# Kernel tuning notes

Measured on AMD Instinct MI355X. Metric: run time of the kernel, lower is better.

Reference implementation:

```python
import jax, jax.numpy as jnp
import numpy as np

B, N, D_V, D_MODEL, D_FF, N_HEADS = 32, 64, 6, 128, 512, 8


def _ln(x, g, b):
    m = x.mean(-1, keepdims=True)
    v = ((x - m) ** 2).mean(-1, keepdims=True)
    return (x - m) / jnp.sqrt(v + 1e-5) * g + b


def _mha(q_in, k_in, v_in, mask, Wq, Wk, Wv, Wo):
    # mask: (b, Lq, Lk) bool, True = attend
    b, Lq, D = q_in.shape
    H, dh = N_HEADS, D_MODEL // N_HEADS
    q = (q_in @ Wq).reshape(b, Lq, H, dh)
    k = (k_in @ Wk).reshape(b, k_in.shape[1], H, dh)
    v = (v_in @ Wv).reshape(b, v_in.shape[1], H, dh)
    s = jnp.einsum('bqhd,bkhd->bhqk', q, k) / (dh ** 0.5)
    s = jnp.where(mask[:, None, :, :], s, -1e9)
    o = jnp.einsum('bhqk,bkhd->bqhd', jax.nn.softmax(s, axis=-1), v).reshape(b, Lq, D)
    return o @ Wo


def setup_inputs() -> dict:
    key = jax.random.key(0)
    ks = jax.random.split(key, 40)
    def p(i, shape, scale=0.05):
        return jax.random.normal(ks[i], shape, dtype=jnp.float32) * scale
    nm = jax.random.randint(ks[1], (B, N, N), 0, 2, dtype=jnp.int32)
    nm = nm.at[:, jnp.arange(N), jnp.arange(N)].set(1)  # self always a neighbor
    inp = {
        'agent_infos': jax.random.normal(ks[0], (B, N, N, D_V), dtype=jnp.float32),
        'neighbor_masks': nm,
        'padding_mask': jnp.ones((B, N), dtype=jnp.int32),
        'is_from_my_env': jnp.ones((B,), dtype=jnp.int32),
        # src_embed
        'W_emb': p(2, (D_V, D_MODEL)), 'b_emb': jnp.zeros((D_MODEL,), jnp.float32),
        # encoder layer (self-attn + FFN, post-LN)
        'Wq': p(3, (D_MODEL, D_MODEL)), 'Wk': p(4, (D_MODEL, D_MODEL)),
        'Wv': p(5, (D_MODEL, D_MODEL)), 'Wo': p(6, (D_MODEL, D_MODEL)),
        'ln1_g': jnp.ones((D_MODEL,), jnp.float32), 'ln1_b': jnp.zeros((D_MODEL,), jnp.float32),
        'W1': p(7, (D_MODEL, D_FF)), 'b1': jnp.zeros((D_FF,), jnp.float32),
        'W2': p(8, (D_FF, D_MODEL)), 'b2': jnp.zeros((D_MODEL,), jnp.float32),
        'ln2_g': jnp.ones((D_MODEL,), jnp.float32), 'ln2_b': jnp.zeros((D_MODEL,), jnp.float32),
        # decoder layer (cross-attn + FFN, post-LN)
        'Uq': p(9, (D_MODEL, D_MODEL)), 'Uk': p(10, (D_MODEL, D_MODEL)),
        'Uv': p(11, (D_MODEL, D_MODEL)), 'Uo': p(12, (D_MODEL, D_MODEL)),
        'ln3_g': jnp.ones((D_MODEL,), jnp.float32), 'ln3_b': jnp.zeros((D_MODEL,), jnp.float32),
        'W3': p(13, (D_MODEL, D_FF)), 'b3': jnp.zeros((D_FF,), jnp.float32),
        'W4': p(14, (D_FF, D_MODEL)), 'b4': jnp.zeros((D_MODEL,), jnp.float32),
        'ln4_g': jnp.ones((D_MODEL,), jnp.float32), 'ln4_b': jnp.zeros((D_MODEL,), jnp.float32),
        # generator (single-head query/key scorer)
        'Wg_q': p(15, (D_MODEL, D_MODEL)), 'Wg_k': p(16, (D_MODEL, D_MODEL)),
    }
    return inp


def reference(agent_infos, neighbor_masks, padding_mask, is_from_my_env,
              W_emb, b_emb, Wq, Wk, Wv, Wo, ln1_g, ln1_b, W1, b1, W2, b2, ln2_g, ln2_b,
              Uq, Uk, Uv, Uo, ln3_g, ln3_b, W3, b3, W4, b4, ln4_g, ln4_b, Wg_q, Wg_k):
    # Fold the per-agent python loop of the original into the batch dim: BN = B * N.
    src = agent_infos.reshape(B * N, N, D_V)
    neigh = neighbor_masks.reshape(B * N, N) != 0           # True = neighbor (attendable)
    x = src @ W_emb + b_emb                                 # (BN, N, D)
    src_mask = neigh[:, :, None] & neigh[:, None, :]        # (BN, N, N)
    x = _ln(x + _mha(x, x, x, src_mask, Wq, Wk, Wv, Wo), ln1_g, ln1_b)
    x = _ln(x + (jax.nn.relu(x @ W1 + b1) @ W2 + b2), ln2_g, ln2_b)
    # context vector -- faithful to the original get_context_vector (which sums rows
    # where pad_tokens==True, i.e. NON-neighbors, and divides by the neighbor count)
    pad = (~neigh)[:, :, None].astype(x.dtype)
    cnt = neigh.sum(axis=1).reshape(-1, 1, 1).astype(x.dtype)
    h_c = (x * pad).sum(axis=1, keepdims=True) / cnt        # (BN, 1, D)
    stm = neigh[:, None, :]                                 # src_tgt_mask (BN, 1, N)
    y = _ln(h_c + _mha(h_c, x, x, stm, Uq, Uk, Uv, Uo), ln3_g, ln3_b)
    y = _ln(y + (jax.nn.relu(y @ W3 + b3) @ W4 + b4), ln4_g, ln4_b)
    logits = jnp.einsum('bqd,bkd->bqk', y @ Wg_q, x @ Wg_k) / (D_MODEL ** 0.5)
    probs = jnp.where(stm, jax.nn.sigmoid(logits), 0.0)[:, 0, :]   # (BN, N)
    att_scores = probs.reshape(B, N, N)
    num_agents = padding_mask.sum(axis=1).astype(x.dtype).reshape(B, 1, 1)
    avg_h_c_N = h_c.reshape(B, N, D_MODEL).sum(axis=1, keepdims=True) / num_agents
    return att_scores, avg_h_c_N
```

## Files before the change

### kernel.cpp

```cpp
#include <hip/hip_runtime.h>
#include <hip/hip_bf16.h>
#include <math.h>

#define ITEMS 2048
#define SEQ   64
#define DM    128
#define DFF   512
#define ATT_OFF 131072

typedef unsigned short u16;
typedef __attribute__((ext_vector_type(4))) unsigned short ushort4v;
typedef __attribute__((ext_vector_type(8))) short short8v;
typedef __attribute__((ext_vector_type(4))) float float4v;

#define MFMA16(a,b,c) __builtin_amdgcn_mfma_f32_16x16x32_bf16(a,b,c,0,0,0)

#define XST 136
#define VST 72
#define PST 76

#define XS_B   0
#define QS_B   17408
#define KS_B   34816
#define VT_B   52224
#define PL_B   70656
#define ZB_B   80384
#define PF_B   80400
#define CNT_B  80656
#define NA_B   80660
#define NB_B   80664
#define ARENA_SZ 80672

#define HC_B   (KS_B+0)
#define QV_B   (KS_B+512)
#define OV_B   (KS_B+1024)
#define YV_B   (KS_B+1536)
#define Y2_B   (KS_B+2048)
#define GW_B   (KS_B+2560)
#define WALL_B (VT_B+0)
#define SALL_B (VT_B+4096)
#define PALL_B (VT_B+6144)
#define TALL_B (VT_B+8192)
#define FF_B   (VT_B+12288)
#define W4P_B  (VT_B+14336)

#define WQ_O   0
#define WK_O   16384
#define WV_O   32768
#define WO_O   49152
#define UK_O   65536
#define UV_O   81920
#define W1_O   98304
#define W2_O   163840
#define UQ_O   229376
#define UO_O   245760
#define WGQ_O  262144
#define WGK_O  278528
#define W3_O   294912
#define W4_O   360448
#define WS_TOT 425984

__device__ __forceinline__ u16 f2b(float f){
  union { float f; unsigned u; } v; v.f = f;
  unsigned r = (v.u + 0x7fffu + ((v.u >> 16) & 1u)) >> 16;
  return (u16)r;
}
__device__ __forceinline__ float b2f(u16 h){
  union { unsigned u; float f; } v; v.u = ((unsigned)h) << 16;
  return v.f;
}
__device__ __forceinline__ float wsum(float v){
  #pragma unroll
  for (int off = 1; off < 64; off <<= 1) v += __shfl_xor(v, off);
  return v;
}
__device__ __forceinline__ void ln_vec(float* v, const float* g, const float* b, int lane){
  float v0 = v[lane], v1 = v[lane+64];
  float m  = wsum(v0+v1) * (1.f/128.f);
  float d0 = v0-m, d1 = v1-m;
  float var = wsum(d0*d0+d1*d1) * (1.f/128.f);
  float inv = rsqrtf(var + 1e-5f);
  v[lane]    = d0*inv*g[lane]    + b[lane];
  v[lane+64] = d1*inv*g[lane+64] + b[lane+64];
}
__device__ __forceinline__ float dot128(const u16* __restrict__ wrow, const float* __restrict__ x){
  const short8v* wr = (const short8v*)wrow;
  float a = 0.f;
  #pragma unroll
  for (int c8 = 0; c8 < 16; c8++){
    short8v v = wr[c8];
    #pragma unroll
    for (int q = 0; q < 8; q++) a += b2f((u16)v[q]) * x[c8*8+q];
  }
  return a;
}

__global__ void prep_all(const float* __restrict__ Wq, const float* __restrict__ Wk,
                         const float* __restrict__ Wv, const float* __restrict__ Wo,
                         const float* __restrict__ Uk, const float* __restrict__ Uv,
                         const float* __restrict__ W1, const float* __restrict__ W2,
                         const float* __restrict__ Uq, const float* __restrict__ Uo,
                         const float* __restrict__ Wgq, const float* __restrict__ Wgk,
                         const float* __restrict__ W3, const float* __restrict__ W4,
                         u16* __restrict__ wts){
  int idx = blockIdx.x*256 + threadIdx.x;
  if (idx >= WS_TOT) return;
  float v;
  if (idx < 98304){
    int wsel = idx >> 14, r = idx & 16383;
    const float* tab[6] = {Wq,Wk,Wv,Wo,Uk,Uv};
    int o = r >> 7, i = r & 127;
    v = tab[wsel][i*128 + o];
  } else if (idx < W2_O){
    int r = idx - W1_O; int o = r >> 7, i = r & 127;
    v = W1[i*512 + o];
  } else if (idx < UQ_O){
    int r = idx - W2_O; int o = r >> 9, i = r & 511;
    v = W2[i*128 + o];
  } else if (idx < UO_O){
    int r = idx - UQ_O; int o = r >> 7, i = r & 127;
    v = Uq[i*128 + o];
  } else if (idx < WGQ_O){
    int r = idx - UO_O; int o = r >> 7, i = r & 127;
    v = Uo[i*128 + o];
  } else if (idx < WGK_O){
    int r = idx - WGQ_O; int o = r >> 7, i = r & 127;
    v = Wgq[i*128 + o];
  } else if (idx < W3_O){
    v = Wgk[idx - WGK_O];
  } else if (idx < W4_O){
    int r = idx - W3_O; int j = r >> 7, e = r & 127;
    v = W3[e*512 + j];
  } else {
    int r = idx - W4_O; int o = r >> 9, j = r & 511;
    v = W4[j*128 + o];
  }
  wts[idx] = f2b(v);
}

__global__ void init_avg(float* __restrict__ out){
  out[ATT_OFF + blockIdx.x*256 + threadIdx.x] = 0.f;
}

__global__ __launch_bounds__(256, 2) void vicsek_fused(
    const float* __restrict__ agent_infos,
    const int*   __restrict__ nmask,
    const int*   __restrict__ pmask,
    const u16*   __restrict__ wts,
    const float* __restrict__ W_emb, const float* __restrict__ b_emb,
    const float* __restrict__ ln1g,  const float* __restrict__ ln1b,
    const float* __restrict__ b1,    const float* __restrict__ b2,
    const float* __restrict__ ln2g,  const float* __restrict__ ln2b,
    const float* __restrict__ ln3g,  const float* __restrict__ ln3b,
    const float* __restrict__ b3,    const float* __restrict__ b4,
    const float* __restrict__ ln4g,  const float* __restrict__ ln4b,
    float* __restrict__ out)
{
  __shared__ __align__(16) char arena[ARENA_SZ];
  u16* Xs = (u16*)(arena + XS_B);
  u16* Qs = (u16*)(arena + QS_B);
  u16* Ks = (u16*)(arena + KS_B);
  u16* VT = (u16*)(arena + VT_B);
  u16* Pl = (u16*)(arena + PL_B);
  u16* zb = (u16*)(arena + ZB_B);
  float* padf  = (float*)(arena + PF_B);
  float* cnt_s = (float*)(arena + CNT_B);
  float* na_s  = (float*)(arena + NA_B);
  unsigned long long* nb_s = (unsigned long long*)(arena + NB_B);

  const int item = blockIdx.x;
  const int tid  = threadIdx.x;
  const int lane = tid & 63;
  const int w    = tid >> 6;
  const int row0 = w*16;
  const int arow = lane & 15;
  const int akg  = lane >> 4;

  const u16* WqT = wts + WQ_O;  const u16* WkT = wts + WK_O;
  const u16* WvT = wts + WV_O;  const u16* WoT = wts + WO_O;
  const u16* UkT = wts + UK_O;  const u16* UvT = wts + UV_O;
  const u16* W1T = wts + W1_O;  const u16* W2T = wts + W2_O;
  const u16* UqT = wts + UQ_O;  const u16* UoT = wts + UO_O;
  const u16* WgqT = wts + WGQ_O; const u16* WgkB = wts + WGK_O;
  const u16* W3T = wts + W3_O;  const u16* W4T = wts + W4_O;

  if (w == 0){
    int m = nmask[item*SEQ + lane];
    padf[lane] = m ? 0.f : 1.f;
    float c = wsum(m ? 1.f : 0.f);
    unsigned long long bb = __ballot(m != 0);
    if (lane == 0){ cnt_s[0] = c; nb_s[0] = bb; }
  }
  if (w == 1){
    float na = wsum((float)pmask[(item>>6)*SEQ + lane]);
    if (lane == 0) na_s[0] = na;
  }
  if (tid < 8) zb[tid] = 0;

  const float* src = agent_infos + (size_t)item*SEQ*6;
  for (int e = tid; e < SEQ*DM; e += 256){
    int r = e >> 7, c = e & 127;
    float a = b_emb[c];
    #pragma unroll
    for (int k = 0; k < 6; k++) a += src[r*6+k]*W_emb[k*DM+c];
    Xs[r*XST + c] = f2b(a);
  }
  __syncthreads();

  const unsigned long long nbits = nb_s[0];

  short8v aX[4];
  #pragma unroll
  for (int k = 0; k < 4; k++) aX[k] = *(const short8v*)(Xs + (row0+arow)*XST + k*32 + akg*8);

  for (int t = 0; t < 8; t++){
    const u16* wq = WqT + (t*16+arow)*128 + akg*8;
    const u16* wk = WkT + (t*16+arow)*128 + akg*8;
    const u16* wv = WvT + (t*16+arow)*128 + akg*8;
    float4v cq = {0,0,0,0}, ck = {0,0,0,0}, cv = {0,0,0,0};
    #pragma unroll
    for (int k = 0; k < 4; k++){
      cq = MFMA16(aX[k], *(const short8v*)(wq + k*32), cq);
      ck = MFMA16(aX[k], *(const short8v*)(wk + k*32), ck);
      cv = MFMA16(*(const short8v*)(wv + k*32), aX[k], cv);
    }
    #pragma unroll
    for (int i = 0; i < 4; i++){
      Qs[(row0+akg*4+i)*XST + t*16+arow] = f2b(cq[i]);
      Ks[(row0+akg*4+i)*XST + t*16+arow] = f2b(ck[i]);
      VT[(t*16+akg*4+i)*VST + row0+arow] = f2b(cv[i]);
    }
  }
  float4v accW[8];
  #pragma unroll
  for (int t = 0; t < 8; t++)
    #pragma unroll
    for (int i = 0; i < 4; i++)
      accW[t][i] = b2f(Xs[(row0+akg*4+i)*XST + t*16 + arow]);
  __syncthreads();

  for (int h = 0; h < 8; h++){
    const u16* qp = (akg < 2) ? (Qs + (row0+arow)*XST + h*16 + akg*8) : zb;
    short8v bq = *(const short8v*)qp;
    float4v st[4];
    #pragma unroll
    for (int kb = 0; kb < 4; kb++){
      const u16* kp = (akg < 2) ? (Ks + (kb*16+arow)*XST + h*16 + akg*8) : zb;
      float4v z = {0,0,0,0};
      st[kb] = MFMA16(*(const short8v*)kp, bq, z);
    }
    bool qok = (nbits >> (row0+arow)) & 1ull;
    float pr[16]; float mx = -3.0e38f;
    #pragma unroll
    for (int kb = 0; kb < 4; kb++)
      #pragma unroll
      for (int i = 0; i < 4; i++){
        int key = kb*16 + akg*4 + i;
        float s = st[kb][i]*0.25f;
        if (!qok || !((nbits>>key)&1ull)) s = -1.0e9f;
        pr[kb*4+i] = s; mx = fmaxf(mx, s);
      }
    mx = fmaxf(mx, __shfl_xor(mx,16)); mx = fmaxf(mx, __shfl_xor(mx,32));
    float sum = 0.f;
    #pragma unroll
    for (int z = 0; z < 16; z++){ pr[z] = __expf(pr[z]-mx); sum += pr[z]; }
    sum += __shfl_xor(sum,16); sum += __shfl_xor(sum,32);
    float inv = 1.f/sum;
    #pragma unroll
    for (int kb = 0; kb < 4; kb++)
      #pragma unroll
      for (int i = 0; i < 4; i++)
        Pl[(kb*16+akg*4+i)*PST + row0+arow] = f2b(pr[kb*4+i]*inv);
    float4v ot = {0,0,0,0};
    #pragma unroll
    for (int c2 = 0; c2 < 2; c2++){
      short8v av = *(const short8v*)(VT + (h*16+arow)*VST + c2*32 + akg*8);
      short8v bp;
      #pragma unroll
      for (int j = 0; j < 8; j++) bp[j] = (short)Pl[(c2*32+akg*8+j)*PST + row0+arow];
      ot = MFMA16(av, bp, ot);
    }
    ushort4v ov4;
    #pragma unroll
    for (int i = 0; i < 4; i++) ov4[i] = f2b(ot[i]);
    *(ushort4v*)(Xs + (row0+arow)*XST + h*16 + akg*4) = ov4;
  }

  {
    short8v aO[4];
    #pragma unroll
    for (int k = 0; k < 4; k++) aO[k] = *(const short8v*)(Xs + (row0+arow)*XST + k*32 + akg*8);
    #pragma unroll
    for (int k = 0; k < 4; k++)
      #pragma unroll
      for (int t = 0; t < 8; t++)
        accW[t] = MFMA16(aO[k], *(const short8v*)(WoT + (t*16+arow)*128 + k*32 + akg*8), accW[t]);
    float g8[8], bb8[8];
    #pragma unroll
    for (int t = 0; t < 8; t++){ g8[t] = ln1g[t*16+arow]; bb8[t] = ln1b[t*16+arow]; }
    #pragma unroll
    for (int i = 0; i < 4; i++){
      float sm = 0.f;
      #pragma unroll
      for (int t = 0; t < 8; t++) sm += accW[t][i];
      sm += __shfl_xor(sm,1); sm += __shfl_xor(sm,2); sm += __shfl_xor(sm,4); sm += __shfl_xor(sm,8);
      float mean = sm*(1.f/128.f);
      float vs = 0.f;
      #pragma unroll
      for (int t = 0; t < 8; t++){ float d = accW[t][i]-mean; vs += d*d; }
      vs += __shfl_xor(vs,1); vs += __shfl_xor(vs,2); vs += __shfl_xor(vs,4); vs += __shfl_xor(vs,8);
      float inv = rsqrtf(vs*(1.f/128.f) + 1e-5f);
      #pragma unroll
      for (int t = 0; t < 8; t++)
        Xs[(row0+akg*4+i)*XST + t*16 + arow] = f2b((accW[t][i]-mean)*inv*g8[t] + bb8[t]);
    }
  }
  #pragma unroll
  for (int k = 0; k < 4; k++) aX[k] = *(const short8v*)(Xs + (row0+arow)*XST + k*32 + akg*8);

  {
    u16* Hb = Qs;
    float4v accY[8];
    #pragma unroll
    for (int t = 0; t < 8; t++){
      float bb = b2[t*16 + arow];
      #pragma unroll
      for (int i = 0; i < 4; i++)
        accY[t][i] = bb + b2f(Xs[(row0+akg*4+i)*XST + t*16 + arow]);
    }
    for (int c = 0; c < 4; c++){
      #pragma unroll
      for (int t = 0; t < 8; t++){
        float bb = b1[c*128 + t*16 + arow];
        float4v acc = {bb,bb,bb,bb};
        #pragma unroll
        for (int k = 0; k < 4; k++)
          acc = MFMA16(aX[k], *(const short8v*)(W1T + (c*128+t*16+arow)*128 + k*32 + akg*8), acc);
        #pragma unroll
        for (int i = 0; i < 4; i++)
          Hb[(row0+akg*4+i)*XST + t*16 + arow] = f2b(fmaxf(acc[i], 0.f));
      }
      #pragma unroll
      for (int k = 0; k < 4; k++){
        short8v aH = *(const short8v*)(Hb + (row0+arow)*XST + k*32 + akg*8);
        #pragma unroll
        for (int t = 0; t < 8; t++)
          accY[t] = MFMA16(aH, *(const short8v*)(W2T + (t*16+arow)*512 + c*128 + k*32 + akg*8), accY[t]);
      }
    }
    float g8[8], bb8[8];
    #pragma unroll
    for (int t = 0; t < 8; t++){ g8[t] = ln2g[t*16+arow]; bb8[t] = ln2b[t*16+arow]; }
    #pragma unroll
    for (int i = 0; i < 4; i++){
      float sm = 0.f;
      #pragma unroll
      for (int t = 0; t < 8; t++) sm += accY[t][i];
      sm += __shfl_xor(sm,1); sm += __shfl_xor(sm,2); sm += __shfl_xor(sm,4); sm += __shfl_xor(sm,8);
      float mean = sm*(1.f/128.f);
      float vs = 0.f;
      #pragma unroll
      for (int t = 0; t < 8; t++){ float d = accY[t][i]-mean; vs += d*d; }
      vs += __shfl_xor(vs,1); vs += __shfl_xor(vs,2); vs += __shfl_xor(vs,4); vs += __shfl_xor(vs,8);
      float inv = rsqrtf(vs*(1.f/128.f) + 1e-5f);
      #pragma unroll
      for (int t = 0; t < 8; t++)
        Xs[(row0+akg*4+i)*XST + t*16 + arow] = f2b((accY[t][i]-mean)*inv*g8[t] + bb8[t]);
    }
  }
  __syncthreads();

  float* hc   = (float*)(arena + HC_B);
  float* qv   = (float*)(arena + QV_B);
  float* ov   = (float*)(arena + OV_B);
  float* yv   = (float*)(arena + YV_B);
  float* y2   = (float*)(arena + Y2_B);
  float* gw   = (float*)(arena + GW_B);
  float* wall = (float*)(arena + WALL_B);
  float* sall = (float*)(arena + SALL_B);
  float* pall = (float*)(arena + PALL_B);
  float* tall = (float*)(arena + TALL_B);
  float* ff   = (float*)(arena + FF_B);
  float* w4p  = (float*)(arena + W4P_B);

  if (tid < DM){
    float a = 0.f;
    #pragma unroll 8
    for (int r = 0; r < SEQ; r++) a += b2f(Xs[r*XST + tid]) * padf[r];
    a /= cnt_s[0];
    hc[tid] = a;
    atomicAdd(&out[ATT_OFF + (item>>6)*DM + tid], a/na_s[0]);
  }
  __syncthreads();

  if (tid < DM) qv[tid] = dot128(UqT + tid*128, hc);
  __syncthreads();
  if (tid < DM){
    #pragma unroll
    for (int h = 0; h < 8; h++){
      float a = 0.f;
      #pragma unroll
      for (int d = 0; d < 16; d++) a += b2f(UkT[(h*16+d)*128 + tid]) * qv[h*16+d];
      wall[h*128 + tid] = a;
    }
  }
  __syncthreads();
  for (int idx = tid; idx < 512; idx += 256){
    int h = idx >> 6, j = idx & 63;
    const short8v* xr = (const short8v*)(Xs + j*XST);
    const float* wv_ = wall + h*128;
    float a = 0.f;
    #pragma unroll
    for (int c8 = 0; c8 < 16; c8++){
      short8v v = xr[c8];
      #pragma unroll
      for (int q = 0; q < 8; q++) a += b2f((u16)v[q]) * wv_[c8*8+q];
    }
    sall[idx] = a*0.25f;
  }
  __syncthreads();
  for (int hh = w; hh < 8; hh += 4){
    float s = sall[hh*64 + lane];
    if (!((nbits>>lane)&1ull)) s = -1.0e9f;
    float mxx = s;
    #pragma unroll
    for (int off = 1; off < 64; off <<= 1) mxx = fmaxf(mxx, __shfl_xor(mxx, off));
    float p = __expf(s - mxx);
    float su = wsum(p);
    pall[hh*64 + lane] = p/su;
  }
  __syncthreads();
  {
    int task = tid >> 1, jh = tid & 1;
    int h = task >> 4, c8 = task & 15;
    float acc8[8] = {0,0,0,0,0,0,0,0};
    #pragma unroll 4
    for (int jj = 0; jj < 32; jj++){
      int j = jh*32 + jj;
      short8v v = *(const short8v*)(Xs + j*XST + c8*8);
      float pj = pall[h*64 + j];
      #pragma unroll
      for (int q = 0; q < 8; q++) acc8[q] += pj * b2f((u16)v[q]);
    }
    #pragma unroll
    for (int q = 0; q < 8; q++) acc8[q] += __shfl_xor(acc8[q], 1);
    if (jh == 0){
      #pragma unroll
      for (int q = 0; q < 8; q++) tall[h*128 + c8*8 + q] = acc8[q];
    }
  }
  __syncthreads();
  if (tid < DM) ov[tid] = dot128(UvT + tid*128, tall + (tid>>4)*128);
  __syncthreads();
  if (tid < DM) yv[tid] = hc[tid] + dot128(UoT + tid*128, ov);
  __syncthreads();
  if (w == 0) ln_vec(yv, ln3g, ln3b, lane);
  __syncthreads();

  for (int j = tid; j < DFF; j += 256)
    ff[j] = fmaxf(b3[j] + dot128(W3T + j*128, yv), 0.f);
  __syncthreads();
  {
    int o = tid & 127, half = tid >> 7;
    const short8v* wr = (const short8v*)(W4T + o*512 + half*256);
    const float* fh = ff + half*256;
    float a = 0.f;
    #pragma unroll
    for (int c8 = 0; c8 < 32; c8++){
      short8v v = wr[c8];
      #pragma unroll
      for (int q = 0; q < 8; q++) a += b2f((u16)v[q]) * fh[c8*8+q];
    }
    w4p[tid] = a;
  }
  __syncthreads();
  if (tid < DM) y2[tid] = b4[tid] + yv[tid] + w4p[tid] + w4p[tid+128];
  __syncthreads();
  if (w == 0) ln_vec(y2, ln4g, ln4b, lane);
  __syncthreads();

  if (tid < DM) qv[tid] = dot128(WgqT + tid*128, y2);
  __syncthreads();
  if (tid < DM) gw[tid] = dot128(WgkB + tid*128, qv);
  __syncthreads();
  if (tid < SEQ){
    float a = dot128(Xs + tid*XST, gw) ;
    a *= 0.08838834764831845f;
    out[(size_t)item*SEQ + tid] = ((nbits>>tid)&1ull) ? (1.f/(1.f+__expf(-a))) : 0.f;
  }
}

extern "C" void kernel_launch(void* const* d_in, const int* in_sizes, int n_in,
                              void* d_out, int out_size, void* d_ws, size_t ws_size,
                              hipStream_t stream)
{
  const float* agent_infos = (const float*)d_in[0];
  const int*   nmask       = (const int*)  d_in[1];
  const int*   pmask       = (const int*)  d_in[2];
  const float* W_emb = (const float*)d_in[4];
  const float* b_emb = (const float*)d_in[5];
  const float* Wq    = (const float*)d_in[6];
  const float* Wk    = (const float*)d_in[7];
  const float* Wv    = (const float*)d_in[8];
  const float* Wo    = (const float*)d_in[9];
  const float* ln1g  = (const float*)d_in[10];
  const float* ln1b  = (const float*)d_in[11];
  const float* W1    = (const float*)d_in[12];
  const float* b1    = (const float*)d_in[13];
  const float* W2    = (const float*)d_in[14];
  const float* b2    = (const float*)d_in[15];
  const float* ln2g  = (const float*)d_in[16];
  const float* ln2b  = (const float*)d_in[17];
  const float* Uq    = (const float*)d_in[18];
  const float* Uk    = (const float*)d_in[19];
  const float* Uv    = (const float*)d_in[20];
  const float* Uo    = (const float*)d_in[21];
  const float* ln3g  = (const float*)d_in[22];
  const float* ln3b  = (const float*)d_in[23];
  const float* W3    = (const float*)d_in[24];
  const float* b3    = (const float*)d_in[25];
  const float* W4    = (const float*)d_in[26];
  const float* b4    = (const float*)d_in[27];
  const float* ln4g  = (const float*)d_in[28];
  const float* ln4b  = (const float*)d_in[29];
  const float* Wgq   = (const float*)d_in[30];
  const float* Wgk   = (const float*)d_in[31];

  float* out = (float*)d_out;
  u16*   wts = (u16*)d_ws;

  prep_all<<<(WS_TOT+255)/256, 256, 0, stream>>>(Wq, Wk, Wv, Wo, Uk, Uv, W1, W2,
                                                 Uq, Uo, Wgq, Wgk, W3, W4, wts);
  init_avg<<<16, 256, 0, stream>>>(out);
  vicsek_fused<<<ITEMS, 256, 0, stream>>>(
      agent_infos, nmask, pmask, wts, W_emb, b_emb,
      ln1g, ln1b, b1, b2, ln2g, ln2b, ln3g, ln3b,
      b3, b4, ln4g, ln4b, out);
}
```

Measured before the change: 636.1 us.

## Repartition GEMMs by output columns per wave and shrink LDS for higher occupancy

Each wave now owns a slice of output columns across all 64 rows instead of a 16-row slice across all columns. Weight fragments are loaded once into registers and reused across the four row groups, which cuts repeated global/L2 weight reads. Attention runs in two batches of four heads with smaller Q/K/V staging buffers, so the LDS arena shrinks and launch bounds rise to 4 blocks per CU. The cost is extra __syncthreads, LayerNorm moved to a separate bf16 round-trip through LDS (adding rounding before normalisation), and tighter register limits that could cause spills.

```diff
diff --git a/kernel.cpp b/kernel.cpp
--- a/kernel.cpp
+++ b/kernel.cpp
@@ -9,40 +9,41 @@
 #define ATT_OFF 131072
 
 typedef unsigned short u16;
-typedef __attribute__((ext_vector_type(4))) unsigned short ushort4v;
 typedef __attribute__((ext_vector_type(8))) short short8v;
 typedef __attribute__((ext_vector_type(4))) float float4v;
 
 #define MFMA16(a,b,c) __builtin_amdgcn_mfma_f32_16x16x32_bf16(a,b,c,0,0,0)
 
-#define XST 136
-#define VST 72
-#define PST 76
+#define XST  136
+#define QST4 68
+#define VST4 70
+#define PST  76
 
 #define XS_B   0
-#define QS_B   17408
-#define KS_B   34816
-#define VT_B   52224
-#define PL_B   70656
-#define ZB_B   80384
-#define PF_B   80400
-#define CNT_B  80656
-#define NA_B   80660
-#define NB_B   80664
-#define ARENA_SZ 80672
-
-#define HC_B   (KS_B+0)
-#define QV_B   (KS_B+512)
-#define OV_B   (KS_B+1024)
-#define YV_B   (KS_B+1536)
-#define Y2_B   (KS_B+2048)
-#define GW_B   (KS_B+2560)
-#define WALL_B (VT_B+0)
-#define SALL_B (VT_B+4096)
-#define PALL_B (VT_B+6144)
-#define TALL_B (VT_B+8192)
-#define FF_B   (VT_B+12288)
-#define W4P_B  (VT_B+14336)
+#define Q4_B   17408
+#define K4_B   26112
+#define V4_B   34816
+#define PL_B   43776
+#define ZB_B   53504
+#define PF_B   53520
+#define NB_B   53776
+#define CNT_B  53784
+#define NA_B   53788
+#define ARENA_SZ 53792
+
+#define CB_B   Q4_B
+#define HC_B   17408
+#define QV_B   17920
+#define OV_B   18432
+#define YV_B   18944
+#define Y2_B   19456
+#define GW_B   19968
+#define WALL_B 20480
+#define SALL_B 24576
+#define PALL_B 26624
+#define TALL_B 28672
+#define FF_B   32768
+#define W4P_B  34816
 
 #define WQ_O   0
 #define WK_O   16384
@@ -142,7 +143,7 @@
   out[ATT_OFF + blockIdx.x*256 + threadIdx.x] = 0.f;
 }
 
-__global__ __launch_bounds__(256, 2) void vicsek_fused(
+__global__ __launch_bounds__(256, 4) void vicsek_fused(
     const float* __restrict__ agent_infos,
     const int*   __restrict__ nmask,
     const int*   __restrict__ pmask,
@@ -158,9 +159,10 @@
 {
   __shared__ __align__(16) char arena[ARENA_SZ];
   u16* Xs = (u16*)(arena + XS_B);
-  u16* Qs = (u16*)(arena + QS_B);
-  u16* Ks = (u16*)(arena + KS_B);
-  u16* VT = (u16*)(arena + VT_B);
+  u16* Q4 = (u16*)(arena + Q4_B);
+  u16* K4 = (u16*)(arena + K4_B);
+  u16* V4 = (u16*)(arena + V4_B);
+  u16* Cb = (u16*)(arena + CB_B);
   u16* Pl = (u16*)(arena + PL_B);
   u16* zb = (u16*)(arena + ZB_B);
   float* padf  = (float*)(arena + PF_B);
@@ -209,164 +211,229 @@
 
   const unsigned long long nbits = nb_s[0];
 
-  short8v aX[4];
+  float4v accW[2][4];
   #pragma unroll
-  for (int k = 0; k < 4; k++) aX[k] = *(const short8v*)(Xs + (row0+arow)*XST + k*32 + akg*8);
-
-  for (int t = 0; t < 8; t++){
-    const u16* wq = WqT + (t*16+arow)*128 + akg*8;
-    const u16* wk = WkT + (t*16+arow)*128 + akg*8;
-    const u16* wv = WvT + (t*16+arow)*128 + akg*8;
-    float4v cq = {0,0,0,0}, ck = {0,0,0,0}, cv = {0,0,0,0};
+  for (int tt = 0; tt < 2; tt++)
+    #pragma unroll
+    for (int rg = 0; rg < 4; rg++)
+      #pragma unroll
+      for (int i = 0; i < 4; i++)
+        accW[tt][rg][i] = b2f(Xs[(rg*16+akg*4+i)*XST + (2*w+tt)*16 + arow]);
+
+  auto stage_batch = [&](int b){
+    int hh = 4*b + w;
+    short8v bq[4], bk[4], bv[4];
     #pragma unroll
     for (int k = 0; k < 4; k++){
-      cq = MFMA16(aX[k], *(const short8v*)(wq + k*32), cq);
-      ck = MFMA16(aX[k], *(const short8v*)(wk + k*32), ck);
-      cv = MFMA16(*(const short8v*)(wv + k*32), aX[k], cv);
-    }
-    #pragma unroll
-    for (int i = 0; i < 4; i++){
-      Qs[(row0+akg*4+i)*XST + t*16+arow] = f2b(cq[i]);
-      Ks[(row0+akg*4+i)*XST + t*16+arow] = f2b(ck[i]);
-      VT[(t*16+akg*4+i)*VST + row0+arow] = f2b(cv[i]);
-    }
-  }
-  float4v accW[8];
+      bq[k] = *(const short8v*)(WqT + (hh*16+arow)*128 + k*32 + akg*8);
+      bk[k] = *(const short8v*)(WkT + (hh*16+arow)*128 + k*32 + akg*8);
+      bv[k] = *(const short8v*)(WvT + (hh*16+arow)*128 + k*32 + akg*8);
+    }
+    #pragma unroll
+    for (int rg = 0; rg < 4; rg++){
+      float4v cq = {0,0,0,0}, ck = {0,0,0,0}, cv = {0,0,0,0};
+      #pragma unroll
+      for (int k = 0; k < 4; k++){
+        short8v a = *(const short8v*)(Xs + (rg*16+arow)*XST + k*32 + akg*8);
+        cq = MFMA16(a, bq[k], cq);
+        ck = MFMA16(a, bk[k], ck);
+        cv = MFMA16(a, bv[k], cv);
+      }
+      #pragma unroll
+      for (int i = 0; i < 4; i++){
+        int r = rg*16 + akg*4 + i;
+        Q4[r*QST4 + w*16 + arow] = f2b(cq[i]);
+        K4[r*QST4 + w*16 + arow] = f2b(ck[i]);
+        V4[r*VST4 + w*16 + arow] = f2b(cv[i]);
+      }
+    }
+  };
+
+  auto heads_batch = [&](float4v* ocp){
+    #pragma unroll
+    for (int l = 0; l < 4; l++){
+      const u16* qp = (akg < 2) ? (Q4 + (row0+arow)*QST4 + l*16 + akg*8) : zb;
+      short8v bq = *(const short8v*)qp;
+      float4v st[4];
+      #pragma unroll
+      for (int kb = 0; kb < 4; kb++){
+        const u16* kp = (akg < 2) ? (K4 + (kb*16+arow)*QST4 + l*16 + akg*8) : zb;
+        float4v z = {0,0,0,0};
+        st[kb] = MFMA16(*(const short8v*)kp, bq, z);
+      }
+      bool qok = (nbits >> (row0+arow)) & 1ull;
+      float pr[16]; float mx = -3.0e38f;
+      #pragma unroll
+      for (int kb = 0; kb < 4; kb++)
+        #pragma unroll
+        for (int i = 0; i < 4; i++){
+          int key = kb*16 + akg*4 + i;
+          float s = st[kb][i]*0.25f;
+          if (!qok || !((nbits>>key)&1ull)) s = -1.0e9f;
+          pr[kb*4+i] = s; mx = fmaxf(mx, s);
+        }
+      mx = fmaxf(mx, __shfl_xor(mx,16)); mx = fmaxf(mx, __shfl_xor(mx,32));
+      float sum = 0.f;
+      #pragma unroll
+      for (int z2 = 0; z2 < 16; z2++){ pr[z2] = __expf(pr[z2]-mx); sum += pr[z2]; }
+      sum += __shfl_xor(sum,16); sum += __shfl_xor(sum,32);
+      float inv = 1.f/sum;
+      #pragma unroll
+      for (int kb = 0; kb < 4; kb++)
+        #pragma unroll
+        for (int i = 0; i < 4; i++)
+          Pl[(kb*16+akg*4+i)*PST + row0+arow] = f2b(pr[kb*4+i]*inv);
+      float4v o = {0,0,0,0};
+      #pragma unroll
+      for (int c2 = 0; c2 < 2; c2++){
+        short8v pa, bv;
+        #pragma unroll
+        for (int j = 0; j < 8; j++){
+          int key = c2*32 + akg*8 + j;
+          pa[j] = (short)Pl[key*PST + row0+arow];
+          bv[j] = (short)V4[key*VST4 + l*16 + arow];
+        }
+        o = MFMA16(pa, bv, o);
+      }
+      ocp[l] = o;
+    }
+  };
+
+  float4v ocA[4], ocB[4];
+  stage_batch(0);
+  __syncthreads();
+  heads_batch(ocA);
+  __syncthreads();
+  stage_batch(1);
+  __syncthreads();
   #pragma unroll
-  for (int t = 0; t < 8; t++)
+  for (int l = 0; l < 4; l++)
     #pragma unroll
     for (int i = 0; i < 4; i++)
-      accW[t][i] = b2f(Xs[(row0+akg*4+i)*XST + t*16 + arow]);
-  __syncthreads();
-
-  for (int h = 0; h < 8; h++){
-    const u16* qp = (akg < 2) ? (Qs + (row0+arow)*XST + h*16 + akg*8) : zb;
-    short8v bq = *(const short8v*)qp;
-    float4v st[4];
-    #pragma unroll
-    for (int kb = 0; kb < 4; kb++){
-      const u16* kp = (akg < 2) ? (Ks + (kb*16+arow)*XST + h*16 + akg*8) : zb;
-      float4v z = {0,0,0,0};
-      st[kb] = MFMA16(*(const short8v*)kp, bq, z);
-    }
-    bool qok = (nbits >> (row0+arow)) & 1ull;
-    float pr[16]; float mx = -3.0e38f;
-    #pragma unroll
-    for (int kb = 0; kb < 4; kb++)
-      #pragma unroll
-      for (int i = 0; i < 4; i++){
-        int key = kb*16 + akg*4 + i;
-        float s = st[kb][i]*0.25f;
-        if (!qok || !((nbits>>key)&1ull)) s = -1.0e9f;
-        pr[kb*4+i] = s; mx = fmaxf(mx, s);
+      Xs[(row0+akg*4+i)*XST + l*16 + arow] = f2b(ocA[l][i]);
+  heads_batch(ocB);
+  #pragma unroll
+  for (int l = 0; l < 4; l++)
+    #pragma unroll
+    for (int i = 0; i < 4; i++)
+      Xs[(row0+akg*4+i)*XST + (4+l)*16 + arow] = f2b(ocB[l][i]);
+  __syncthreads();
+
+  {
+    short8v bWo[2][4];
+    #pragma unroll
+    for (int tt = 0; tt < 2; tt++)
+      #pragma unroll
+      for (int k = 0; k < 4; k++)
+        bWo[tt][k] = *(const short8v*)(WoT + ((2*w+tt)*16+arow)*128 + k*32 + akg*8);
+    #pragma unroll
+    for (int k = 0; k < 4; k++)
+      #pragma unroll
+      for (int rg = 0; rg < 4; rg++){
+        short8v a = *(const short8v*)(Xs + (rg*16+arow)*XST + k*32 + akg*8);
+        #pragma unroll
+        for (int tt = 0; tt < 2; tt++)
+          accW[tt][rg] = MFMA16(a, bWo[tt][k], accW[tt][rg]);
       }
-    mx = fmaxf(mx, __shfl_xor(mx,16)); mx = fmaxf(mx, __shfl_xor(mx,32));
-    float sum = 0.f;
-    #pragma unroll
-    for (int z = 0; z < 16; z++){ pr[z] = __expf(pr[z]-mx); sum += pr[z]; }
-    sum += __shfl_xor(sum,16); sum += __shfl_xor(sum,32);
-    float inv = 1.f/sum;
-    #pragma unroll
-    for (int kb = 0; kb < 4; kb++)
-      #pragma unroll
-      for (int i = 0; i < 4; i++)
-        Pl[(kb*16+akg*4+i)*PST + row0+arow] = f2b(pr[kb*4+i]*inv);
-    float4v ot = {0,0,0,0};
-    #pragma unroll
-    for (int c2 = 0; c2 < 2; c2++){
-      short8v av = *(const short8v*)(VT + (h*16+arow)*VST + c2*32 + akg*8);
-      short8v bp;
-      #pragma unroll
-      for (int j = 0; j < 8; j++) bp[j] = (short)Pl[(c2*32+akg*8+j)*PST + row0+arow];
-      ot = MFMA16(av, bp, ot);
-    }
-    ushort4v ov4;
-    #pragma unroll
-    for (int i = 0; i < 4; i++) ov4[i] = f2b(ot[i]);
-    *(ushort4v*)(Xs + (row0+arow)*XST + h*16 + akg*4) = ov4;
-  }
+    #pragma unroll
+    for (int tt = 0; tt < 2; tt++)
+      #pragma unroll
+      for (int rg = 0; rg < 4; rg++)
+        #pragma unroll
+        for (int i = 0; i < 4; i++)
+          Cb[(rg*16+akg*4+i)*XST + (2*w+tt)*16 + arow] = f2b(accW[tt][rg][i]);
+  }
+  __syncthreads();
+  for (int rr = 0; rr < 16; rr++){
+    int r = row0 + rr;
+    float v0 = b2f(Cb[r*XST+lane]), v1 = b2f(Cb[r*XST+lane+64]);
+    float m  = wsum(v0+v1) * (1.f/128.f);
+    float d0 = v0-m, d1 = v1-m;
+    float var = wsum(d0*d0+d1*d1) * (1.f/128.f);
+    float inv = rsqrtf(var + 1e-5f);
+    Xs[r*XST+lane]    = f2b(d0*inv*ln1g[lane]    + ln1b[lane]);
+    Xs[r*XST+lane+64] = f2b(d1*inv*ln1g[lane+64] + ln1b[lane+64]);
+  }
+  __syncthreads();
 
   {
-    short8v aO[4];
-    #pragma unroll
-    for (int k = 0; k < 4; k++) aO[k] = *(const short8v*)(Xs + (row0+arow)*XST + k*32 + akg*8);
-    #pragma unroll
-    for (int k = 0; k < 4; k++)
-      #pragma unroll
-      for (int t = 0; t < 8; t++)
-        accW[t] = MFMA16(aO[k], *(const short8v*)(WoT + (t*16+arow)*128 + k*32 + akg*8), accW[t]);
-    float g8[8], bb8[8];
-    #pragma unroll
-    for (int t = 0; t < 8; t++){ g8[t] = ln1g[t*16+arow]; bb8[t] = ln1b[t*16+arow]; }
-    #pragma unroll
-    for (int i = 0; i < 4; i++){
-      float sm = 0.f;
-      #pragma unroll
-      for (int t = 0; t < 8; t++) sm += accW[t][i];
-      sm += __shfl_xor(sm,1); sm += __shfl_xor(sm,2); sm += __shfl_xor(sm,4); sm += __shfl_xor(sm,8);
-      float mean = sm*(1.f/128.f);
-      float vs = 0.f;
-      #pragma unroll
-      for (int t = 0; t < 8; t++){ float d = accW[t][i]-mean; vs += d*d; }
-      vs += __shfl_xor(vs,1); vs += __shfl_xor(vs,2); vs += __shfl_xor(vs,4); vs += __shfl_xor(vs,8);
-      float inv = rsqrtf(vs*(1.f/128.f) + 1e-5f);
-      #pragma unroll
-      for (int t = 0; t < 8; t++)
-        Xs[(row0+akg*4+i)*XST + t*16 + arow] = f2b((accW[t][i]-mean)*inv*g8[t] + bb8[t]);
-    }
-  }
-  #pragma unroll
-  for (int k = 0; k < 4; k++) aX[k] = *(const short8v*)(Xs + (row0+arow)*XST + k*32 + akg*8);
-
-  {
-    u16* Hb = Qs;
-    float4v accY[8];
-    #pragma unroll
-    for (int t = 0; t < 8; t++){
-      float bb = b2[t*16 + arow];
-      #pragma unroll
-      for (int i = 0; i < 4; i++)
-        accY[t][i] = bb + b2f(Xs[(row0+akg*4+i)*XST + t*16 + arow]);
+    u16* Hb = Cb;
+    float4v accY[2][4];
+    #pragma unroll
+    for (int tt = 0; tt < 2; tt++){
+      float bb = b2[(2*w+tt)*16 + arow];
+      #pragma unroll
+      for (int rg = 0; rg < 4; rg++)
+        #pragma unroll
+        for (int i = 0; i < 4; i++)
+          accY[tt][rg][i] = bb + b2f(Xs[(rg*16+akg*4+i)*XST + (2*w+tt)*16 + arow]);
     }
     for (int c = 0; c < 4; c++){
-      #pragma unroll
-      for (int t = 0; t < 8; t++){
-        float bb = b1[c*128 + t*16 + arow];
-        float4v acc = {bb,bb,bb,bb};
+      short8v bW1[2][4];
+      #pragma unroll
+      for (int tt = 0; tt < 2; tt++)
         #pragma unroll
         for (int k = 0; k < 4; k++)
-          acc = MFMA16(aX[k], *(const short8v*)(W1T + (c*128+t*16+arow)*128 + k*32 + akg*8), acc);
+          bW1[tt][k] = *(const short8v*)(W1T + (c*128 + w*32 + tt*16 + arow)*128 + k*32 + akg*8);
+      float4v hid[2][4];
+      #pragma unroll
+      for (int tt = 0; tt < 2; tt++){
+        float bb = b1[c*128 + w*32 + tt*16 + arow];
+        #pragma unroll
+        for (int rg = 0; rg < 4; rg++){ hid[tt][rg][0]=bb; hid[tt][rg][1]=bb; hid[tt][rg][2]=bb; hid[tt][rg][3]=bb; }
+      }
+      #pragma unroll
+      for (int k = 0; k < 4; k++)
+        #pragma unroll
+        for (int rg = 0; rg < 4; rg++){
+          short8v a = *(const short8v*)(Xs + (rg*16+arow)*XST + k*32 + akg*8);
+          #pragma unroll
+          for (int tt = 0; tt < 2; tt++)
+            hid[tt][rg] = MFMA16(a, bW1[tt][k], hid[tt][rg]);
+        }
+      #pragma unroll
+      for (int tt = 0; tt < 2; tt++)
+        #pragma unroll
+        for (int rg = 0; rg < 4; rg++)
+          #pragma unroll
+          for (int i = 0; i < 4; i++)
+            Hb[(rg*16+akg*4+i)*XST + w*32 + tt*16 + arow] = f2b(fmaxf(hid[tt][rg][i], 0.f));
+      __syncthreads();
+      short8v bW2[2][4];
+      #pragma unroll
+      for (int tt = 0; tt < 2; tt++)
+        #pragma unroll
+        for (int k = 0; k < 4; k++)
+          bW2[tt][k] = *(const short8v*)(W2T + (w*32 + tt*16 + arow)*512 + c*128 + k*32 + akg*8);
+      #pragma unroll
+      for (int k = 0; k < 4; k++)
+        #pragma unroll
+        for (int rg = 0; rg < 4; rg++){
+          short8v aH = *(const short8v*)(Hb + (rg*16+arow)*XST + k*32 + akg*8);
+          #pragma unroll
+          for (int tt = 0; tt < 2; tt++)
+            accY[tt][rg] = MFMA16(aH, bW2[tt][k], accY[tt][rg]);
+        }
+      __syncthreads();
+    }
+    #pragma unroll
+    for (int tt = 0; tt < 2; tt++)
+      #pragma unroll
+      for (int rg = 0; rg < 4; rg++)
         #pragma unroll
         for (int i = 0; i < 4; i++)
-          Hb[(row0+akg*4+i)*XST + t*16 + arow] = f2b(fmaxf(acc[i], 0.f));
-      }
-      #pragma unroll
-      for (int k = 0; k < 4; k++){
-        short8v aH = *(const short8v*)(Hb + (row0+arow)*XST + k*32 + akg*8);
-        #pragma unroll
-        for (int t = 0; t < 8; t++)
-          accY[t] = MFMA16(aH, *(const short8v*)(W2T + (t*16+arow)*512 + c*128 + k*32 + akg*8), accY[t]);
-      }
-    }
-    float g8[8], bb8[8];
-    #pragma unroll
-    for (int t = 0; t < 8; t++){ g8[t] = ln2g[t*16+arow]; bb8[t] = ln2b[t*16+arow]; }
-    #pragma unroll
-    for (int i = 0; i < 4; i++){
-      float sm = 0.f;
-      #pragma unroll
-      for (int t = 0; t < 8; t++) sm += accY[t][i];
-      sm += __shfl_xor(sm,1); sm += __shfl_xor(sm,2); sm += __shfl_xor(sm,4); sm += __shfl_xor(sm,8);
-      float mean = sm*(1.f/128.f);
-      float vs = 0.f;
-      #pragma unroll
-      for (int t = 0; t < 8; t++){ float d = accY[t][i]-mean; vs += d*d; }
-      vs += __shfl_xor(vs,1); vs += __shfl_xor(vs,2); vs += __shfl_xor(vs,4); vs += __shfl_xor(vs,8);
-      float inv = rsqrtf(vs*(1.f/128.f) + 1e-5f);
-      #pragma unroll
-      for (int t = 0; t < 8; t++)
-        Xs[(row0+akg*4+i)*XST + t*16 + arow] = f2b((accY[t][i]-mean)*inv*g8[t] + bb8[t]);
-    }
+          Cb[(rg*16+akg*4+i)*XST + (2*w+tt)*16 + arow] = f2b(accY[tt][rg][i]);
+  }
+  __syncthreads();
+  for (int rr = 0; rr < 16; rr++){
+    int r = row0 + rr;
+    float v0 = b2f(Cb[r*XST+lane]), v1 = b2f(Cb[r*XST+lane+64]);
+    float m  = wsum(v0+v1) * (1.f/128.f);
+    float d0 = v0-m, d1 = v1-m;
+    float var = wsum(d0*d0+d1*d1) * (1.f/128.f);
+    float inv = rsqrtf(var + 1e-5f);
+    Xs[r*XST+lane]    = f2b(d0*inv*ln2g[lane]    + ln2b[lane]);
+    Xs[r*XST+lane+64] = f2b(d1*inv*ln2g[lane+64] + ln2b[lane+64]);
   }
   __syncthreads();
 
@@ -484,7 +551,7 @@
   if (tid < DM) gw[tid] = dot128(WgkB + tid*128, qv);
   __syncthreads();
   if (tid < SEQ){
-    float a = dot128(Xs + tid*XST, gw) ;
+    float a = dot128(Xs + tid*XST, gw);
     a *= 0.08838834764831845f;
     out[(size_t)item*SEQ + tid] = ((nbits>>tid)&1ull) ? (1.f/(1.f+__expf(-a))) : 0.f;
   }
```

Measured after the change: 722.7 us. 13.6% more time.

## Split self-attention QKV staging into two head batches to shrink LDS and raise occupancy

Applied to the files above, without the earlier changes.

The Q/K/V projection now runs in two batches of four heads. Each batch is staged into smaller LDS buffers and attended before the next batch is computed. This roughly cuts the shared-memory arena from about 80KB to about 54KB, so launch bounds can ask for 3 blocks per CU instead of 2. The cost is two extra block-wide barriers, a tighter register budget, and overlaid scratch offsets that could alias if any are wrong.

```diff
diff --git a/kernel.cpp b/kernel.cpp
--- a/kernel.cpp
+++ b/kernel.cpp
@@ -15,34 +15,36 @@
 
 #define MFMA16(a,b,c) __builtin_amdgcn_mfma_f32_16x16x32_bf16(a,b,c,0,0,0)
 
-#define XST 136
-#define VST 72
-#define PST 76
+#define XST  136
+#define QST4 72
+#define VST4 72
+#define PST  68
 
 #define XS_B   0
-#define QS_B   17408
-#define KS_B   34816
-#define VT_B   52224
-#define PL_B   70656
-#define ZB_B   80384
-#define PF_B   80400
-#define CNT_B  80656
-#define NA_B   80660
-#define NB_B   80664
-#define ARENA_SZ 80672
-
-#define HC_B   (KS_B+0)
-#define QV_B   (KS_B+512)
-#define OV_B   (KS_B+1024)
-#define YV_B   (KS_B+1536)
-#define Y2_B   (KS_B+2048)
-#define GW_B   (KS_B+2560)
-#define WALL_B (VT_B+0)
-#define SALL_B (VT_B+4096)
-#define PALL_B (VT_B+6144)
-#define TALL_B (VT_B+8192)
-#define FF_B   (VT_B+12288)
-#define W4P_B  (VT_B+14336)
+#define Q4_B   17408
+#define K4_B   26624
+#define V4_B   35840
+#define PL_B   45056
+#define ZB_B   53760
+#define PF_B   53776
+#define NB_B   54032
+#define CNT_B  54040
+#define NA_B   54044
+#define ARENA_SZ 54048
+
+#define HB_B   Q4_B
+#define HC_B   17408
+#define QV_B   17920
+#define OV_B   18432
+#define YV_B   18944
+#define Y2_B   19456
+#define GW_B   19968
+#define WALL_B 20480
+#define SALL_B 24576
+#define PALL_B 26624
+#define TALL_B 28672
+#define FF_B   35840
+#define W4P_B  37888
 
 #define WQ_O   0
 #define WK_O   16384
@@ -142,7 +144,7 @@
   out[ATT_OFF + blockIdx.x*256 + threadIdx.x] = 0.f;
 }
 
-__global__ __launch_bounds__(256, 2) void vicsek_fused(
+__global__ __launch_bounds__(256, 3) void vicsek_fused(
     const float* __restrict__ agent_infos,
     const int*   __restrict__ nmask,
     const int*   __restrict__ pmask,
@@ -157,12 +159,12 @@
     float* __restrict__ out)
 {
   __shared__ __align__(16) char arena[ARENA_SZ];
-  u16* Xs = (u16*)(arena + XS_B);
-  u16* Qs = (u16*)(arena + QS_B);
-  u16* Ks = (u16*)(arena + KS_B);
-  u16* VT = (u16*)(arena + VT_B);
-  u16* Pl = (u16*)(arena + PL_B);
-  u16* zb = (u16*)(arena + ZB_B);
+  u16* Xs  = (u16*)(arena + XS_B);
+  u16* Q4  = (u16*)(arena + Q4_B);
+  u16* K4  = (u16*)(arena + K4_B);
+  u16* VT4 = (u16*)(arena + V4_B);
+  u16* Pl  = (u16*)(arena + PL_B);
+  u16* zb  = (u16*)(arena + ZB_B);
   float* padf  = (float*)(arena + PF_B);
   float* cnt_s = (float*)(arena + CNT_B);
   float* na_s  = (float*)(arena + NA_B);
@@ -213,78 +215,94 @@
   #pragma unroll
   for (int k = 0; k < 4; k++) aX[k] = *(const short8v*)(Xs + (row0+arow)*XST + k*32 + akg*8);
 
-  for (int t = 0; t < 8; t++){
-    const u16* wq = WqT + (t*16+arow)*128 + akg*8;
-    const u16* wk = WkT + (t*16+arow)*128 + akg*8;
-    const u16* wv = WvT + (t*16+arow)*128 + akg*8;
-    float4v cq = {0,0,0,0}, ck = {0,0,0,0}, cv = {0,0,0,0};
-    #pragma unroll
-    for (int k = 0; k < 4; k++){
-      cq = MFMA16(aX[k], *(const short8v*)(wq + k*32), cq);
-      ck = MFMA16(aX[k], *(const short8v*)(wk + k*32), ck);
-      cv = MFMA16(*(const short8v*)(wv + k*32), aX[k], cv);
-    }
-    #pragma unroll
-    for (int i = 0; i < 4; i++){
-      Qs[(row0+akg*4+i)*XST + t*16+arow] = f2b(cq[i]);
-      Ks[(row0+akg*4+i)*XST + t*16+arow] = f2b(ck[i]);
-      VT[(t*16+akg*4+i)*VST + row0+arow] = f2b(cv[i]);
-    }
-  }
   float4v accW[8];
   #pragma unroll
   for (int t = 0; t < 8; t++)
     #pragma unroll
     for (int i = 0; i < 4; i++)
       accW[t][i] = b2f(Xs[(row0+akg*4+i)*XST + t*16 + arow]);
-  __syncthreads();
-
-  for (int h = 0; h < 8; h++){
-    const u16* qp = (akg < 2) ? (Qs + (row0+arow)*XST + h*16 + akg*8) : zb;
-    short8v bq = *(const short8v*)qp;
-    float4v st[4];
-    #pragma unroll
-    for (int kb = 0; kb < 4; kb++){
-      const u16* kp = (akg < 2) ? (Ks + (kb*16+arow)*XST + h*16 + akg*8) : zb;
-      float4v z = {0,0,0,0};
-      st[kb] = MFMA16(*(const short8v*)kp, bq, z);
-    }
-    bool qok = (nbits >> (row0+arow)) & 1ull;
-    float pr[16]; float mx = -3.0e38f;
-    #pragma unroll
-    for (int kb = 0; kb < 4; kb++)
+
+  auto stage_batch = [&](int b){
+    #pragma unroll
+    for (int l = 0; l < 4; l++){
+      int hh = 4*b + l;
+      const u16* wq = WqT + (hh*16+arow)*128 + akg*8;
+      const u16* wk = WkT + (hh*16+arow)*128 + akg*8;
+      const u16* wv = WvT + (hh*16+arow)*128 + akg*8;
+      float4v cq = {0,0,0,0}, ck = {0,0,0,0}, cv = {0,0,0,0};
+      #pragma unroll
+      for (int k = 0; k < 4; k++){
+        cq = MFMA16(aX[k], *(const short8v*)(wq + k*32), cq);
+        ck = MFMA16(aX[k], *(const short8v*)(wk + k*32), ck);
+        cv = MFMA16(*(const short8v*)(wv + k*32), aX[k], cv);
+      }
       #pragma unroll
       for (int i = 0; i < 4; i++){
-        int key = kb*16 + akg*4 + i;
-        float s = st[kb][i]*0.25f;
-        if (!qok || !((nbits>>key)&1ull)) s = -1.0e9f;
-        pr[kb*4+i] = s; mx = fmaxf(mx, s);
+        Q4[(row0+akg*4+i)*QST4 + l*16+arow] = f2b(cq[i]);
+        K4[(row0+akg*4+i)*QST4 + l*16+arow] = f2b(ck[i]);
+        VT4[(l*16+akg*4+i)*VST4 + row0+arow] = f2b(cv[i]);
       }
-    mx = fmaxf(mx, __shfl_xor(mx,16)); mx = fmaxf(mx, __shfl_xor(mx,32));
-    float sum = 0.f;
-    #pragma unroll
-    for (int z = 0; z < 16; z++){ pr[z] = __expf(pr[z]-mx); sum += pr[z]; }
-    sum += __shfl_xor(sum,16); sum += __shfl_xor(sum,32);
-    float inv = 1.f/sum;
-    #pragma unroll
-    for (int kb = 0; kb < 4; kb++)
-      #pragma unroll
-      for (int i = 0; i < 4; i++)
-        Pl[(kb*16+akg*4+i)*PST + row0+arow] = f2b(pr[kb*4+i]*inv);
-    float4v ot = {0,0,0,0};
-    #pragma unroll
-    for (int c2 = 0; c2 < 2; c2++){
-      short8v av = *(const short8v*)(VT + (h*16+arow)*VST + c2*32 + akg*8);
-      short8v bp;
-      #pragma unroll
-      for (int j = 0; j < 8; j++) bp[j] = (short)Pl[(c2*32+akg*8+j)*PST + row0+arow];
-      ot = MFMA16(av, bp, ot);
-    }
-    ushort4v ov4;
-    #pragma unroll
-    for (int i = 0; i < 4; i++) ov4[i] = f2b(ot[i]);
-    *(ushort4v*)(Xs + (row0+arow)*XST + h*16 + akg*4) = ov4;
-  }
+    }
+  };
+
+  auto attend_batch = [&](int b){
+    #pragma unroll
+    for (int l = 0; l < 4; l++){
+      const u16* qp = (akg < 2) ? (Q4 + (row0+arow)*QST4 + l*16 + akg*8) : zb;
+      short8v bq = *(const short8v*)qp;
+      float4v st[4];
+      #pragma unroll
+      for (int kb = 0; kb < 4; kb++){
+        const u16* kp = (akg < 2) ? (K4 + (kb*16+arow)*QST4 + l*16 + akg*8) : zb;
+        float4v z = {0,0,0,0};
+        st[kb] = MFMA16(*(const short8v*)kp, bq, z);
+      }
+      bool qok = (nbits >> (row0+arow)) & 1ull;
+      float pr[16]; float mx = -3.0e38f;
+      #pragma unroll
+      for (int kb = 0; kb < 4; kb++)
+        #pragma unroll
+        for (int i = 0; i < 4; i++){
+          int key = kb*16 + akg*4 + i;
+          float s = st[kb][i]*0.25f;
+          if (!qok || !((nbits>>key)&1ull)) s = -1.0e9f;
+          pr[kb*4+i] = s; mx = fmaxf(mx, s);
+        }
+      mx = fmaxf(mx, __shfl_xor(mx,16)); mx = fmaxf(mx, __shfl_xor(mx,32));
+      float sum = 0.f;
+      #pragma unroll
+      for (int z2 = 0; z2 < 16; z2++){ pr[z2] = __expf(pr[z2]-mx); sum += pr[z2]; }
+      sum += __shfl_xor(sum,16); sum += __shfl_xor(sum,32);
+      float inv = 1.f/sum;
+      #pragma unroll
+      for (int kb = 0; kb < 4; kb++)
+        #pragma unroll
+        for (int i = 0; i < 4; i++)
+          Pl[(kb*16+akg*4+i)*PST + row0+arow] = f2b(pr[kb*4+i]*inv);
+      float4v ot = {0,0,0,0};
+      #pragma unroll
+      for (int c2 = 0; c2 < 2; c2++){
+        short8v av = *(const short8v*)(VT4 + (l*16+arow)*VST4 + c2*32 + akg*8);
+        short8v bp;
+        #pragma unroll
+        for (int j = 0; j < 8; j++) bp[j] = (short)Pl[(c2*32+akg*8+j)*PST + row0+arow];
+        ot = MFMA16(av, bp, ot);
+      }
+      ushort4v ov4;
+      #pragma unroll
+      for (int i = 0; i < 4; i++) ov4[i] = f2b(ot[i]);
+      *(ushort4v*)(Xs + (row0+arow)*XST + (4*b+l)*16 + akg*4) = ov4;
+    }
+  };
+
+  stage_batch(0);
+  __syncthreads();
+  attend_batch(0);
+  __syncthreads();
+  stage_batch(1);
+  __syncthreads();
+  attend_batch(1);
+  __syncthreads();
 
   {
     short8v aO[4];
@@ -319,7 +337,7 @@
   for (int k = 0; k < 4; k++) aX[k] = *(const short8v*)(Xs + (row0+arow)*XST + k*32 + akg*8);
 
   {
-    u16* Hb = Qs;
+    u16* Hb = (u16*)(arena + HB_B);
     float4v accY[8];
     #pragma unroll
     for (int t = 0; t < 8; t++){
@@ -484,7 +502,7 @@
   if (tid < DM) gw[tid] = dot128(WgkB + tid*128, qv);
   __syncthreads();
   if (tid < SEQ){
-    float a = dot128(Xs + tid*XST, gw) ;
+    float a = dot128(Xs + tid*XST, gw);
     a *= 0.08838834764831845f;
     out[(size_t)item*SEQ + tid] = ((nbits>>tid)&1ull) ? (1.f/(1.f+__expf(-a))) : 0.f;
   }
```

Measured after the change: 654.6 us. +2.9%, slower.
